# Performance work log

Measured on AMD Instinct MI355X. Metric: run time of the kernel, lower is better.

Reference implementation:

```python
import jax, jax.numpy as jnp
import numpy as np

B, T, D_IN, H1, H2, K = 16, 1024, 384, 1024, 1024, 9


def _l2normalize(w, axis):
    # matches F.normalize(w, dim=axis): w / max(||w||_2, 1e-12)
    n = jnp.sqrt(jnp.sum(w * w, axis=axis, keepdims=True))
    return w / jnp.maximum(n, 1e-12)


def _mish(x):
    return x * jnp.tanh(jax.nn.softplus(x))


def setup_inputs() -> dict:
    key = jax.random.key(0)
    ks = jax.random.split(key, 11)
    f32 = jnp.float32
    return {
        "input": jax.random.normal(ks[0], (B, T, D_IN), f32),
        "d_w": jax.random.normal(ks[1], (B, H1, 1, K), f32),
        "d_g": jax.random.normal(ks[2], (B, H1), f32),
        "d_b": jax.random.normal(ks[3], (B, H1), f32),
        "p_w": jax.random.normal(ks[4], (B, H1, H2, 1), f32),
        "p_g": jax.random.normal(ks[5], (B, H1), f32),
        "p_b": jax.random.normal(ks[6], (B, H2), f32),
        "w1_w": jax.random.normal(ks[7], (H1, D_IN), f32) * 0.05,
        "w1_b": jax.random.normal(ks[8], (H1,), f32) * 0.05,
        "w2_w": jax.random.normal(ks[9], (D_IN, H2), f32) * 0.05,
        "w2_b": jax.random.normal(ks[10], (D_IN,), f32) * 0.05,
    }


def reference(input, d_w, d_g, d_b, p_w, p_g, p_b, w1_w, w1_b, w2_w, w2_b):
    residual = input
    # w_1: 1x1 conv == per-position linear, then Mish (dropout = identity in eval)
    h = _mish(jnp.einsum('btc,hc->bth', input, w1_w) + w1_b)   # [B,T,H1]
    x = jnp.transpose(h, (0, 2, 1))                            # [B,H1,T]
    k = d_w.shape[-1]
    pad = (k - 1) // 2
    t = x.shape[-1]
    xp = jnp.pad(x, ((0, 0), (0, 0), (pad, pad)))              # [B,H1,T+2p]
    idx = jnp.arange(t)[:, None] + jnp.arange(k)[None, :]      # [T,K]
    xu = xp[:, :, idx]                                         # [B,H1,T,K] (unfold)
    # weight-normalized dynamic depthwise conv weights
    dwn = _l2normalize(d_w, axis=1) * d_g[:, :, None, None]    # [B,H1,1,K]
    # torch.einsum('bctk,bcwk->bct') with d_w expanded along w(=T): w is summed,
    # and every w-slice is identical, so the dot product picks up a factor of T.
    y = jnp.einsum('bctk,bck->bct', xu, dwn[:, :, 0, :]) * t   # [B,H1,T]
    y = y + d_b[:, :, None]
    # weight-normalized dynamic pointwise mix
    pwn = _l2normalize(p_w, axis=1) * p_g[:, :, None, None]    # [B,H1,H2,1]
    z = jnp.einsum('bct,bco->bot', y, pwn[..., 0])             # [B,H2,T]
    z = z + p_b[:, :, None]
    # w_2: 1x1 conv back to d_in, residual add
    out2 = jnp.einsum('bot,do->btd', z, w2_w) + w2_b           # [B,T,D_IN]
    return out2 + residual
```

## Files before the change

### kernel.cpp

```cpp
#include <hip/hip_runtime.h>

#define BCNT 16
#define TT 1024
#define DIN 384
#define H1 1024
#define H2 1024
#define KW 9

typedef __attribute__((ext_vector_type(8))) short bhalf8;
typedef __attribute__((ext_vector_type(4))) float f32x4;

typedef const __attribute__((address_space(1))) void* gas_ptr;
typedef __attribute__((address_space(3))) void* lds_ptr;

__device__ __forceinline__ float bf2f(unsigned short u) {
    return __uint_as_float(((unsigned int)u) << 16);
}
__device__ __forceinline__ unsigned short f2bf(float f) {
    unsigned int u = __float_as_uint(f);
    unsigned int r = (u + 0x7FFFu + ((u >> 16) & 1u)) >> 16;
    return (unsigned short)r;
}
__device__ __forceinline__ float mish_f(float x) {
    if (x > 20.f) return x;
    float u = __expf(x);
    float n = u * u + 2.f * u;
    return x * n / (n + 2.f);
}


__global__ __launch_bounds__(256) void k_cvt3(
    const float* __restrict__ s0, unsigned short* __restrict__ d0, int n0,
    const float* __restrict__ s1, unsigned short* __restrict__ d1, int n1,
    const float* __restrict__ s2, unsigned short* __restrict__ d2, int n2) {
    int i = blockIdx.x * 256 + threadIdx.x;
    const float* s; unsigned short* d; int j = i;
    if (i < n0) { s = s0; d = d0; }
    else if ((j = i - n0) < n1) { s = s1; d = d1; }
    else if ((j = i - n0 - n1) < n2) { s = s2; d = d2; }
    else return;
    float4 v = ((const float4*)s)[j];
    ushort4 o;
    o.x = f2bf(v.x); o.y = f2bf(v.y); o.z = f2bf(v.z); o.w = f2bf(v.w);
    ((ushort4*)d)[j] = o;
}

__global__ __launch_bounds__(256) void k_zero(float* __restrict__ p, int n) {
    int i = blockIdx.x * 256 + threadIdx.x;
    if (i < n) p[i] = 0.f;
}

__global__ void k_norm_d(const float* __restrict__ d_w, float* __restrict__ norm_d) {
    int idx = blockIdx.x;
    int b = idx / KW, k = idx % KW;
    float s = 0.f;
    for (int c = threadIdx.x; c < H1; c += 256) {
        float v = d_w[((size_t)b * H1 + c) * KW + k];
        s += v * v;
    }
    __shared__ float red[256];
    red[threadIdx.x] = s; __syncthreads();
    for (int st = 128; st > 0; st >>= 1) {
        if (threadIdx.x < st) red[threadIdx.x] += red[threadIdx.x + st];
        __syncthreads();
    }
    if (threadIdx.x == 0) norm_d[idx] = sqrtf(red[0]);
}

__global__ void k_dwn(const float* __restrict__ d_w, const float* __restrict__ d_g,
                      const float* __restrict__ norm_d, float* __restrict__ dwn_s) {
    int i = blockIdx.x * 256 + threadIdx.x;
    int k = i % KW;
    int c = (i / KW) % H1;
    int b = i / (KW * H1);
    float n = fmaxf(norm_d[b * KW + k], 1e-12f);
    dwn_s[i] = d_w[i] / n * d_g[b * H1 + c] * (float)TT;
}

__global__ __launch_bounds__(256) void k_tpw2(const float* __restrict__ p_w,
                                              const float* __restrict__ p_g,
                                              unsigned short* __restrict__ pwTu,
                                              float* __restrict__ sumsq) {
    __shared__ float tile[32][33];
    __shared__ float red[8][32];
    int tx = threadIdx.x & 31, ty = threadIdx.x >> 5;
    int c0 = blockIdx.x * 32, o0 = blockIdx.y * 32, b = blockIdx.z;
    float s = 0.f;
#pragma unroll
    for (int j = 0; j < 4; j++) {
        float v = p_w[((size_t)b * H1 + c0 + ty + j * 8) * H2 + o0 + tx];
        tile[ty + j * 8][tx] = v;
        s += v * v;
    }
    red[ty][tx] = s;
    __syncthreads();
    if (ty == 0) {
        float t = 0.f;
#pragma unroll
        for (int r = 0; r < 8; r++) t += red[r][tx];
        atomicAdd(&sumsq[(size_t)b * H2 + o0 + tx], t);
    }
#pragma unroll
    for (int j = 0; j < 4; j++) {
        int o = o0 + ty + j * 8, c = c0 + tx;
        float v = tile[tx][ty + j * 8] * p_g[(size_t)b * H1 + c];
        pwTu[((size_t)b * H2 + o) * H1 + c] = f2bf(v);
    }
}

__global__ __launch_bounds__(256) void k_inv(const float* __restrict__ sumsq,
                                             float* __restrict__ inv_np, int n) {
    int i = blockIdx.x * 256 + threadIdx.x;
    if (i < n) inv_np[i] = 1.0f / fmaxf(sqrtf(sumsq[i]), 1e-12f);
}

__global__ __launch_bounds__(256) void k_conv(const unsigned short* __restrict__ h,
                                              const float* __restrict__ dwn_s,
                                              const float* __restrict__ d_b,
                                              unsigned short* __restrict__ y) {
    int tid = threadIdx.x;
    int c2 = blockIdx.y * 256 + tid;
    int c = c2 * 2;
    int t0 = blockIdx.x * 64;
    int b = blockIdx.z;
    const ushort2* hb = (const ushort2*)(h + (size_t)b * TT * H1);
    ushort2* yb = (ushort2*)(y + (size_t)b * TT * H1);
    float k0[KW], k1[KW];
#pragma unroll
    for (int i = 0; i < KW; i++) {
        k0[i] = dwn_s[((size_t)b * H1 + c) * KW + i];
        k1[i] = dwn_s[((size_t)b * H1 + c + 1) * KW + i];
    }
    float db0 = d_b[b * H1 + c], db1 = d_b[b * H1 + c + 1];
    float w0[KW], w1[KW];
#pragma unroll
    for (int i = 0; i < 8; i++) {
        int t = t0 - 4 + i;
        if (t >= 0 && t < TT) {
            ushort2 v = hb[(size_t)t * (H1 / 2) + c2];
            w0[i] = bf2f(v.x); w1[i] = bf2f(v.y);
        } else { w0[i] = 0.f; w1[i] = 0.f; }
    }
    for (int j = 0; j < 64; j++) {
        int t = t0 + j;
        int tl = t + 4;
        if (tl < TT) {
            ushort2 v = hb[(size_t)tl * (H1 / 2) + c2];
            w0[8] = bf2f(v.x); w1[8] = bf2f(v.y);
        } else { w0[8] = 0.f; w1[8] = 0.f; }
        float a0 = db0, a1 = db1;
#pragma unroll
        for (int i = 0; i < KW; i++) { a0 += k0[i] * w0[i]; a1 += k1[i] * w1[i]; }
        ushort2 o; o.x = f2bf(a0); o.y = f2bf(a1);
        yb[(size_t)t * (H1 / 2) + c2] = o;
#pragma unroll
        for (int i = 0; i < 8; i++) { w0[i] = w0[i + 1]; w1[i] = w1[i + 1]; }
    }
}

template <int MODE, int SWIZ>
__global__ __launch_bounds__(256, 4) void gemm_nt(
    const unsigned short* __restrict__ A, const unsigned short* __restrict__ Bm,
    void* __restrict__ Cp, int Kdim, int lda, int ldb, int ldc,
    long sA, long sB, long sC,
    const float* __restrict__ bias, int biasStride,
    const float* __restrict__ scale,
    const unsigned short* __restrict__ residbf) {
    __shared__ __attribute__((aligned(16))) unsigned short Al[128 * 32];
    __shared__ __attribute__((aligned(16))) unsigned short Bl[128 * 32];

    const int tid = threadIdx.x;
    const int lane = tid & 63, wv = tid >> 6;

    int bx, by, bz;
    if constexpr (SWIZ) {
        int l = blockIdx.x;
        int xcd = l & 7, s = l >> 3;
        bz = xcd * 2 + (s >> 6);
        int u = s & 63;
        bx = u & 7; by = u >> 3;
    } else {
        bx = blockIdx.x; by = blockIdx.y; bz = blockIdx.z;
    }
    const int bm = bx * 128, bn = by * 128;

    const unsigned short* Ab = A + (size_t)sA * bz;
    const unsigned short* Bb = Bm + (size_t)sB * bz;

    const int rS = lane >> 2;
    const int cS = (((lane & 3) ^ ((rS >> 1) & 3)) & 3) * 8;

    const int wm = (wv >> 1) * 64, wn = (wv & 1) * 64;
    const int l16 = lane & 15, quad = lane >> 4;
    const int fr = (l16 >> 1) & 3;

    f32x4 acc[4][4];
#pragma unroll
    for (int i = 0; i < 4; i++)
#pragma unroll
        for (int j = 0; j < 4; j++)
#pragma unroll
            for (int r = 0; r < 4; r++) acc[i][j][r] = 0.f;

    const int ktiles = Kdim / 32;
    for (int kt = 0; kt < ktiles; ++kt) {
        const int kofs = kt * 32 + cS;
#pragma unroll
        for (int i = 0; i < 2; i++) {
            const int ch = wv + i * 4;
            const unsigned short* ga = Ab + (size_t)(bm + ch * 16 + rS) * lda + kofs;
            __builtin_amdgcn_global_load_lds((gas_ptr)ga, (lds_ptr)&Al[ch * 512], 16, 0, 0);
            const unsigned short* gb = Bb + (size_t)(bn + ch * 16 + rS) * ldb + kofs;
            __builtin_amdgcn_global_load_lds((gas_ptr)gb, (lds_ptr)&Bl[ch * 512], 16, 0, 0);
        }
        __syncthreads();

        bhalf8 af[4], bf[4];
#pragma unroll
        for (int mi = 0; mi < 4; mi++)
            af[mi] = *(const bhalf8*)&Al[(wm + mi * 16 + l16) * 32 + ((quad ^ fr) & 3) * 8];
#pragma unroll
        for (int ni = 0; ni < 4; ni++)
            bf[ni] = *(const bhalf8*)&Bl[(wn + ni * 16 + l16) * 32 + ((quad ^ fr) & 3) * 8];
#pragma unroll
        for (int mi = 0; mi < 4; mi++)
#pragma unroll
            for (int ni = 0; ni < 4; ni++)
                acc[mi][ni] = __builtin_amdgcn_mfma_f32_16x16x32_bf16(af[mi], bf[ni],
                                                                     acc[mi][ni], 0, 0, 0);
        __syncthreads();
    }

#pragma unroll
    for (int mi = 0; mi < 4; mi++)
#pragma unroll
        for (int ni = 0; ni < 4; ni++)
#pragma unroll
            for (int r = 0; r < 4; r++) {
                int gm = bm + wm + mi * 16 + quad * 4 + r;
                int gn = bn + wn + ni * 16 + l16;
                float v = acc[mi][ni][r];
                size_t cidx = (size_t)sC * bz + (size_t)gm * ldc + gn;
                if constexpr (MODE == 0) {
                    v = mish_f(v + bias[gn]);
                    ((unsigned short*)Cp)[cidx] = f2bf(v);
                } else if constexpr (MODE == 1) {
                    size_t si = (size_t)bz * biasStride + gn;
                    v = v * scale[si] + bias[si];
                    ((unsigned short*)Cp)[cidx] = f2bf(v);
                } else {
                    v += bias[gn] + bf2f(residbf[cidx]);
                    ((float*)Cp)[cidx] = v;
                }
            }
}


extern "C" void kernel_launch(void* const* d_in, const int* in_sizes, int n_in,
                              void* d_out, int out_size, void* d_ws, size_t ws_size,
                              hipStream_t stream) {
    const float* input = (const float*)d_in[0];
    const float* d_w   = (const float*)d_in[1];
    const float* d_g   = (const float*)d_in[2];
    const float* d_b   = (const float*)d_in[3];
    const float* p_w   = (const float*)d_in[4];
    const float* p_g   = (const float*)d_in[5];
    const float* p_b   = (const float*)d_in[6];
    const float* w1_w  = (const float*)d_in[7];
    const float* w1_b  = (const float*)d_in[8];
    const float* w2_w  = (const float*)d_in[9];
    const float* w2_b  = (const float*)d_in[10];
    float* out = (float*)d_out;

    char* ws = (char*)d_ws;
    size_t off = 0;
    auto alloc = [&](size_t bytes) {
        char* p = ws + off;
        off += (bytes + 255) & ~(size_t)255;
        return p;
    };
    float* norm_d        = (float*)alloc((size_t)BCNT * KW * 4);
    float* dwn_s         = (float*)alloc((size_t)BCNT * H1 * KW * 4);
    float* sumsq         = (float*)alloc((size_t)BCNT * H2 * 4);
    float* inv_np        = (float*)alloc((size_t)BCNT * H2 * 4);
    unsigned short* inbf = (unsigned short*)alloc((size_t)BCNT * TT * DIN * 2);
    unsigned short* w1bf = (unsigned short*)alloc((size_t)H1 * DIN * 2);
    unsigned short* w2bf = (unsigned short*)alloc((size_t)DIN * H2 * 2);
    unsigned short* h    = (unsigned short*)alloc((size_t)BCNT * TT * H1 * 2);
    unsigned short* y    = (unsigned short*)alloc((size_t)BCNT * TT * H1 * 2);
    unsigned short* pwTu = (unsigned short*)alloc((size_t)BCNT * H2 * H1 * 2);
    unsigned short* zt   = (unsigned short*)alloc((size_t)BCNT * TT * H2 * 2);

    const int n4_in = BCNT * TT * DIN / 4, n4_w1 = H1 * DIN / 4, n4_w2 = DIN * H2 / 4;
    k_cvt3<<<(n4_in + n4_w1 + n4_w2 + 255) / 256, 256, 0, stream>>>(
        input, inbf, n4_in, w1_w, w1bf, n4_w1, w2_w, w2bf, n4_w2);

    k_zero<<<(BCNT * H2 + 255) / 256, 256, 0, stream>>>(sumsq, BCNT * H2);
    k_norm_d<<<BCNT * KW, 256, 0, stream>>>(d_w, norm_d);
    k_dwn<<<(BCNT * H1 * KW) / 256, 256, 0, stream>>>(d_w, d_g, norm_d, dwn_s);
    k_tpw2<<<dim3(H1 / 32, H2 / 32, BCNT), 256, 0, stream>>>(p_w, p_g, pwTu, sumsq);
    k_inv<<<(BCNT * H2 + 255) / 256, 256, 0, stream>>>(sumsq, inv_np, BCNT * H2);

    gemm_nt<0, 0><<<dim3(BCNT * TT / 128, H1 / 128, 1), 256, 0, stream>>>(
        inbf, w1bf, h, DIN, DIN, DIN, H1, 0, 0, 0, w1_b, 0, nullptr, nullptr);

    k_conv<<<dim3(TT / 64, H1 / 512, BCNT), 256, 0, stream>>>(h, dwn_s, d_b, y);

    gemm_nt<1, 1><<<dim3(1024, 1, 1), 256, 0, stream>>>(
        y, pwTu, zt, H1, H1, H1, H2, (long)TT * H1, (long)H2 * H1, (long)TT * H2,
        p_b, H2, inv_np, nullptr);

    gemm_nt<2, 0><<<dim3(BCNT * TT / 128, DIN / 128, 1), 256, 0, stream>>>(
        zt, w2bf, out, H2, H2, H2, DIN, 0, 0, 0, w2_b, 0, nullptr, inbf);
}
```

Measured before the change: 289.3 us.

## Double GEMM K-tile to 64, narrow final GEMM tile, fuse small prep kernels

The GEMM now loads a 64-wide K tile per iteration with an 8-way XOR swizzle and runs two MFMA sub-steps per barrier, which halves the number of sync rounds. The GEMM also gains a TN template parameter, and the last GEMM uses 128x64 tiles to put more blocks on a small N. Separately, the zeroing kernel is folded into the convert kernel, the norm and dwn kernels are merged into one, and the inverse-norm kernel is dropped by computing rsqrt in the GEMM epilogue. This removes several launches, at the cost of doubled LDS per block, which may lower occupancy.

```diff
diff --git a/kernel.cpp b/kernel.cpp
--- a/kernel.cpp
+++ b/kernel.cpp
@@ -29,28 +29,28 @@
 }
 
 
-__global__ __launch_bounds__(256) void k_cvt3(
+__global__ __launch_bounds__(256) void k_cvt3z(
     const float* __restrict__ s0, unsigned short* __restrict__ d0, int n0,
     const float* __restrict__ s1, unsigned short* __restrict__ d1, int n1,
-    const float* __restrict__ s2, unsigned short* __restrict__ d2, int n2) {
+    const float* __restrict__ s2, unsigned short* __restrict__ d2, int n2,
+    float* __restrict__ zb, int n3) {
     int i = blockIdx.x * 256 + threadIdx.x;
     const float* s; unsigned short* d; int j = i;
     if (i < n0) { s = s0; d = d0; }
     else if ((j = i - n0) < n1) { s = s1; d = d1; }
     else if ((j = i - n0 - n1) < n2) { s = s2; d = d2; }
-    else return;
+    else if ((j = i - n0 - n1 - n2) < n3) {
+        ((float4*)zb)[j] = make_float4(0.f, 0.f, 0.f, 0.f);
+        return;
+    } else return;
     float4 v = ((const float4*)s)[j];
     ushort4 o;
     o.x = f2bf(v.x); o.y = f2bf(v.y); o.z = f2bf(v.z); o.w = f2bf(v.w);
     ((ushort4*)d)[j] = o;
 }
 
-__global__ __launch_bounds__(256) void k_zero(float* __restrict__ p, int n) {
-    int i = blockIdx.x * 256 + threadIdx.x;
-    if (i < n) p[i] = 0.f;
-}
-
-__global__ void k_norm_d(const float* __restrict__ d_w, float* __restrict__ norm_d) {
+__global__ void k_norm_dwn(const float* __restrict__ d_w, const float* __restrict__ d_g,
+                           float* __restrict__ dwn_s) {
     int idx = blockIdx.x;
     int b = idx / KW, k = idx % KW;
     float s = 0.f;
@@ -59,22 +59,19 @@
         s += v * v;
     }
     __shared__ float red[256];
+    __shared__ float nsh;
     red[threadIdx.x] = s; __syncthreads();
     for (int st = 128; st > 0; st >>= 1) {
         if (threadIdx.x < st) red[threadIdx.x] += red[threadIdx.x + st];
         __syncthreads();
     }
-    if (threadIdx.x == 0) norm_d[idx] = sqrtf(red[0]);
-}
-
-__global__ void k_dwn(const float* __restrict__ d_w, const float* __restrict__ d_g,
-                      const float* __restrict__ norm_d, float* __restrict__ dwn_s) {
-    int i = blockIdx.x * 256 + threadIdx.x;
-    int k = i % KW;
-    int c = (i / KW) % H1;
-    int b = i / (KW * H1);
-    float n = fmaxf(norm_d[b * KW + k], 1e-12f);
-    dwn_s[i] = d_w[i] / n * d_g[b * H1 + c] * (float)TT;
+    if (threadIdx.x == 0) nsh = fmaxf(sqrtf(red[0]), 1e-12f);
+    __syncthreads();
+    float n = nsh;
+    for (int c = threadIdx.x; c < H1; c += 256) {
+        size_t o = ((size_t)b * H1 + c) * KW + k;
+        dwn_s[o] = d_w[o] / n * d_g[b * H1 + c] * (float)TT;
+    }
 }
 
 __global__ __launch_bounds__(256) void k_tpw2(const float* __restrict__ p_w,
@@ -106,12 +103,6 @@
         float v = tile[tx][ty + j * 8] * p_g[(size_t)b * H1 + c];
         pwTu[((size_t)b * H2 + o) * H1 + c] = f2bf(v);
     }
-}
-
-__global__ __launch_bounds__(256) void k_inv(const float* __restrict__ sumsq,
-                                             float* __restrict__ inv_np, int n) {
-    int i = blockIdx.x * 256 + threadIdx.x;
-    if (i < n) inv_np[i] = 1.0f / fmaxf(sqrtf(sumsq[i]), 1e-12f);
 }
 
 __global__ __launch_bounds__(256) void k_conv(const unsigned short* __restrict__ h,
@@ -158,16 +149,17 @@
     }
 }
 
-template <int MODE, int SWIZ>
+template <int MODE, int SWIZ, int TN>
 __global__ __launch_bounds__(256, 4) void gemm_nt(
     const unsigned short* __restrict__ A, const unsigned short* __restrict__ Bm,
     void* __restrict__ Cp, int Kdim, int lda, int ldb, int ldc,
     long sA, long sB, long sC,
     const float* __restrict__ bias, int biasStride,
-    const float* __restrict__ scale,
+    const float* __restrict__ sumsq,
     const unsigned short* __restrict__ residbf) {
-    __shared__ __attribute__((aligned(16))) unsigned short Al[128 * 32];
-    __shared__ __attribute__((aligned(16))) unsigned short Bl[128 * 32];
+    constexpr int WN = TN / 32;
+    __shared__ __attribute__((aligned(16))) unsigned short Al[128 * 64];
+    __shared__ __attribute__((aligned(16))) unsigned short Bl[TN * 64];
 
     const int tid = threadIdx.x;
     const int lane = tid & 63, wv = tid >> 6;
@@ -182,59 +174,67 @@
     } else {
         bx = blockIdx.x; by = blockIdx.y; bz = blockIdx.z;
     }
-    const int bm = bx * 128, bn = by * 128;
+    const int bm = bx * 128, bn = by * TN;
 
     const unsigned short* Ab = A + (size_t)sA * bz;
     const unsigned short* Bb = Bm + (size_t)sB * bz;
 
-    const int rS = lane >> 2;
-    const int cS = (((lane & 3) ^ ((rS >> 1) & 3)) & 3) * 8;
-
-    const int wm = (wv >> 1) * 64, wn = (wv & 1) * 64;
+    const int rS = lane >> 3;
+    const int cS = ((lane & 7) ^ (rS & 7)) * 8;
+
+    const int wm = (wv >> 1) * 64, wn = (wv & 1) * (TN / 2);
     const int l16 = lane & 15, quad = lane >> 4;
-    const int fr = (l16 >> 1) & 3;
-
-    f32x4 acc[4][4];
+    const int fx = l16 & 7;
+
+    f32x4 acc[4][WN];
 #pragma unroll
     for (int i = 0; i < 4; i++)
 #pragma unroll
-        for (int j = 0; j < 4; j++)
+        for (int j = 0; j < WN; j++)
 #pragma unroll
             for (int r = 0; r < 4; r++) acc[i][j][r] = 0.f;
 
-    const int ktiles = Kdim / 32;
+    const int ktiles = Kdim / 64;
     for (int kt = 0; kt < ktiles; ++kt) {
-        const int kofs = kt * 32 + cS;
-#pragma unroll
-        for (int i = 0; i < 2; i++) {
-            const int ch = wv + i * 4;
-            const unsigned short* ga = Ab + (size_t)(bm + ch * 16 + rS) * lda + kofs;
+        const int kofs = kt * 64 + cS;
+#pragma unroll
+        for (int i = 0; i < 4; i++) {
+            const int ch = i * 4 + wv;
+            const unsigned short* ga = Ab + (size_t)(bm + ch * 8 + rS) * lda + kofs;
             __builtin_amdgcn_global_load_lds((gas_ptr)ga, (lds_ptr)&Al[ch * 512], 16, 0, 0);
-            const unsigned short* gb = Bb + (size_t)(bn + ch * 16 + rS) * ldb + kofs;
+        }
+#pragma unroll
+        for (int i = 0; i < TN / 32; i++) {
+            const int ch = i * 4 + wv;
+            const unsigned short* gb = Bb + (size_t)(bn + ch * 8 + rS) * ldb + kofs;
             __builtin_amdgcn_global_load_lds((gas_ptr)gb, (lds_ptr)&Bl[ch * 512], 16, 0, 0);
         }
         __syncthreads();
 
-        bhalf8 af[4], bf[4];
-#pragma unroll
-        for (int mi = 0; mi < 4; mi++)
-            af[mi] = *(const bhalf8*)&Al[(wm + mi * 16 + l16) * 32 + ((quad ^ fr) & 3) * 8];
-#pragma unroll
-        for (int ni = 0; ni < 4; ni++)
-            bf[ni] = *(const bhalf8*)&Bl[(wn + ni * 16 + l16) * 32 + ((quad ^ fr) & 3) * 8];
-#pragma unroll
-        for (int mi = 0; mi < 4; mi++)
-#pragma unroll
-            for (int ni = 0; ni < 4; ni++)
-                acc[mi][ni] = __builtin_amdgcn_mfma_f32_16x16x32_bf16(af[mi], bf[ni],
-                                                                     acc[mi][ni], 0, 0, 0);
+#pragma unroll
+        for (int kk = 0; kk < 2; kk++) {
+            const int cg = ((kk * 4 + quad) ^ fx) * 8;
+            bhalf8 af[4], bf[WN];
+#pragma unroll
+            for (int mi = 0; mi < 4; mi++)
+                af[mi] = *(const bhalf8*)&Al[(wm + mi * 16 + l16) * 64 + cg];
+#pragma unroll
+            for (int ni = 0; ni < WN; ni++)
+                bf[ni] = *(const bhalf8*)&Bl[(wn + ni * 16 + l16) * 64 + cg];
+#pragma unroll
+            for (int mi = 0; mi < 4; mi++)
+#pragma unroll
+                for (int ni = 0; ni < WN; ni++)
+                    acc[mi][ni] = __builtin_amdgcn_mfma_f32_16x16x32_bf16(af[mi], bf[ni],
+                                                                         acc[mi][ni], 0, 0, 0);
+        }
         __syncthreads();
     }
 
 #pragma unroll
     for (int mi = 0; mi < 4; mi++)
 #pragma unroll
-        for (int ni = 0; ni < 4; ni++)
+        for (int ni = 0; ni < WN; ni++)
 #pragma unroll
             for (int r = 0; r < 4; r++) {
                 int gm = bm + wm + mi * 16 + quad * 4 + r;
@@ -246,7 +246,8 @@
                     ((unsigned short*)Cp)[cidx] = f2bf(v);
                 } else if constexpr (MODE == 1) {
                     size_t si = (size_t)bz * biasStride + gn;
-                    v = v * scale[si] + bias[si];
+                    float rr = rsqrtf(fmaxf(sumsq[si], 1e-24f));
+                    v = v * rr + bias[si];
                     ((unsigned short*)Cp)[cidx] = f2bf(v);
                 } else {
                     v += bias[gn] + bf2f(residbf[cidx]);
@@ -279,10 +280,8 @@
         off += (bytes + 255) & ~(size_t)255;
         return p;
     };
-    float* norm_d        = (float*)alloc((size_t)BCNT * KW * 4);
     float* dwn_s         = (float*)alloc((size_t)BCNT * H1 * KW * 4);
     float* sumsq         = (float*)alloc((size_t)BCNT * H2 * 4);
-    float* inv_np        = (float*)alloc((size_t)BCNT * H2 * 4);
     unsigned short* inbf = (unsigned short*)alloc((size_t)BCNT * TT * DIN * 2);
     unsigned short* w1bf = (unsigned short*)alloc((size_t)H1 * DIN * 2);
     unsigned short* w2bf = (unsigned short*)alloc((size_t)DIN * H2 * 2);
@@ -292,24 +291,22 @@
     unsigned short* zt   = (unsigned short*)alloc((size_t)BCNT * TT * H2 * 2);
 
     const int n4_in = BCNT * TT * DIN / 4, n4_w1 = H1 * DIN / 4, n4_w2 = DIN * H2 / 4;
-    k_cvt3<<<(n4_in + n4_w1 + n4_w2 + 255) / 256, 256, 0, stream>>>(
-        input, inbf, n4_in, w1_w, w1bf, n4_w1, w2_w, w2bf, n4_w2);
-
-    k_zero<<<(BCNT * H2 + 255) / 256, 256, 0, stream>>>(sumsq, BCNT * H2);
-    k_norm_d<<<BCNT * KW, 256, 0, stream>>>(d_w, norm_d);
-    k_dwn<<<(BCNT * H1 * KW) / 256, 256, 0, stream>>>(d_w, d_g, norm_d, dwn_s);
+    const int n4_z = BCNT * H2 / 4;
+    k_cvt3z<<<(n4_in + n4_w1 + n4_w2 + n4_z + 255) / 256, 256, 0, stream>>>(
+        input, inbf, n4_in, w1_w, w1bf, n4_w1, w2_w, w2bf, n4_w2, sumsq, n4_z);
+
+    k_norm_dwn<<<BCNT * KW, 256, 0, stream>>>(d_w, d_g, dwn_s);
     k_tpw2<<<dim3(H1 / 32, H2 / 32, BCNT), 256, 0, stream>>>(p_w, p_g, pwTu, sumsq);
-    k_inv<<<(BCNT * H2 + 255) / 256, 256, 0, stream>>>(sumsq, inv_np, BCNT * H2);
-
-    gemm_nt<0, 0><<<dim3(BCNT * TT / 128, H1 / 128, 1), 256, 0, stream>>>(
+
+    gemm_nt<0, 0, 128><<<dim3(BCNT * TT / 128, H1 / 128, 1), 256, 0, stream>>>(
         inbf, w1bf, h, DIN, DIN, DIN, H1, 0, 0, 0, w1_b, 0, nullptr, nullptr);
 
     k_conv<<<dim3(TT / 64, H1 / 512, BCNT), 256, 0, stream>>>(h, dwn_s, d_b, y);
 
-    gemm_nt<1, 1><<<dim3(1024, 1, 1), 256, 0, stream>>>(
+    gemm_nt<1, 1, 128><<<dim3(1024, 1, 1), 256, 0, stream>>>(
         y, pwTu, zt, H1, H1, H1, H2, (long)TT * H1, (long)H2 * H1, (long)TT * H2,
-        p_b, H2, inv_np, nullptr);
-
-    gemm_nt<2, 0><<<dim3(BCNT * TT / 128, DIN / 128, 1), 256, 0, stream>>>(
+        p_b, H2, sumsq, nullptr);
+
+    gemm_nt<2, 0, 64><<<dim3(BCNT * TT / 128, DIN / 64, 1), 256, 0, stream>>>(
         zt, w2bf, out, H2, H2, H2, DIN, 0, 0, 0, w2_b, 0, nullptr, inbf);
 }
```

New measurement: 269.4 us. 6.9% less time.
